# Optimization experiments

Measured on AMD Instinct MI355X. Metric: run time of the kernel, lower is better.

## Reference

```python
import jax, jax.numpy as jnp
import numpy as np

D_MODEL = 1024
HEAD_SIZE = 64

def setup_inputs() -> dict:
    key = jax.random.key(0)
    ks = jax.random.split(key, 7)
    s = 1.0 / np.sqrt(D_MODEL)
    return {
        "x": jax.random.normal(ks[0], (4, 2048, D_MODEL), dtype=jnp.float32),
        "wq": jax.random.uniform(ks[1], (D_MODEL, HEAD_SIZE), jnp.float32, -s, s),
        "bq": jax.random.uniform(ks[2], (HEAD_SIZE,), jnp.float32, -s, s),
        "wk": jax.random.uniform(ks[3], (D_MODEL, HEAD_SIZE), jnp.float32, -s, s),
        "bk": jax.random.uniform(ks[4], (HEAD_SIZE,), jnp.float32, -s, s),
        "wv": jax.random.uniform(ks[5], (D_MODEL, HEAD_SIZE), jnp.float32, -s, s),
        "bv": jax.random.uniform(ks[6], (HEAD_SIZE,), jnp.float32, -s, s),
    }

def reference(x, wq, bq, wk, bk, wv, bv):
    # x: [b, n, d_model]; projections -> [b, n, head_size]
    q = x @ wq + bq
    k = x @ wk + bk
    v = x @ wv + bv
    scores = jnp.einsum("bnd,bmd->bnm", q, k) / jnp.sqrt(jnp.float32(HEAD_SIZE))
    attn = jax.nn.softmax(scores, axis=-1)  # [b, n, n]
    return jnp.einsum("bnm,bmd->bnd", attn, v)
```

## Files before the change

kernel.cpp:

```cpp
#include <hip/hip_runtime.h>
#include <math.h>

#define D_MODEL 1024
#define HEAD 64
#define SEQ 2048
#define BATCH 4

typedef _Float16 f16x4 __attribute__((ext_vector_type(4)));
typedef _Float16 f16x8 __attribute__((ext_vector_type(8)));
typedef float f32x4 __attribute__((ext_vector_type(4)));

__global__ __launch_bounds__(256) void prep_w(
    const float* __restrict__ wq, const float* __restrict__ wk,
    const float* __restrict__ wv, _Float16* __restrict__ wT)
{
    const float* w = (blockIdx.y == 0) ? wq : (blockIdx.y == 1) ? wk : wv;
    const int kbase = blockIdx.x * 64;
    __shared__ float t[64][65];
    const int tid = threadIdx.x;
    #pragma unroll
    for (int i = 0; i < 16; i++) {
        int idx = tid + i * 256;
        int kk = idx >> 6, c = idx & 63;
        t[kk][c] = w[(size_t)(kbase + kk) * 64 + c];
    }
    __syncthreads();
    #pragma unroll
    for (int i = 0; i < 16; i++) {
        int idx = tid + i * 256;
        int c = idx >> 6, kk = idx & 63;
        wT[(size_t)(blockIdx.y * 64 + c) * 1024 + kbase + kk] = (_Float16)t[kk][c];
    }
}

__global__ __launch_bounds__(896, 7) void proj_kernel(
    const float* __restrict__ x, const _Float16* __restrict__ wT,
    const float* __restrict__ bq, const float* __restrict__ bk2,
    const float* __restrict__ bv,
    _Float16* __restrict__ q, _Float16* __restrict__ k, _Float16* __restrict__ vT)
{
    const int tid = threadIdx.x;
    const int wave = tid >> 6;
    const int lane = tid & 63;
    const int l16 = lane & 15;
    const int quad = lane >> 4;
    const int row0 = blockIdx.x * 16;

    __shared__ __align__(16) _Float16 Xs[2][16][136];

    const bool producer = (wave >= 12);

    const int tid2 = tid - 768;
    const int srow = (tid2 >> 3) & 15;
    const int kg = (tid2 & 7) * 16;
    const float* xp = x + (size_t)(row0 + srow) * D_MODEL + kg;

    const _Float16* wp = wT + (size_t)(wave * 16 + l16) * D_MODEL + quad * 8;

    if (producer) {
        float4 f0 = *(const float4*)(xp);
        float4 f1 = *(const float4*)(xp + 4);
        float4 f2 = *(const float4*)(xp + 8);
        float4 f3 = *(const float4*)(xp + 12);
        f16x8 h0, h1;
        h0[0] = (_Float16)f0.x; h0[1] = (_Float16)f0.y;
        h0[2] = (_Float16)f0.z; h0[3] = (_Float16)f0.w;
        h0[4] = (_Float16)f1.x; h0[5] = (_Float16)f1.y;
        h0[6] = (_Float16)f1.z; h0[7] = (_Float16)f1.w;
        h1[0] = (_Float16)f2.x; h1[1] = (_Float16)f2.y;
        h1[2] = (_Float16)f2.z; h1[3] = (_Float16)f2.w;
        h1[4] = (_Float16)f3.x; h1[5] = (_Float16)f3.y;
        h1[6] = (_Float16)f3.z; h1[7] = (_Float16)f3.w;
        *(f16x8*)&Xs[0][srow][kg] = h0;
        *(f16x8*)&Xs[0][srow][kg + 8] = h1;
    }

    f32x4 acc = (f32x4){0.f, 0.f, 0.f, 0.f};

    #pragma unroll 1
    for (int c = 0; c < 8; c++) {
        __syncthreads();
        if (!producer) {
            f16x8 bw0 = *(const f16x8*)(wp + c * 128);
            f16x8 bw1 = *(const f16x8*)(wp + c * 128 + 32);
            f16x8 bw2 = *(const f16x8*)(wp + c * 128 + 64);
            f16x8 bw3 = *(const f16x8*)(wp + c * 128 + 96);
            const int bsel = c & 1;
            f16x8 aX0 = *(const f16x8*)&Xs[bsel][l16][0 * 32 + quad * 8];
            f16x8 aX1 = *(const f16x8*)&Xs[bsel][l16][1 * 32 + quad * 8];
            f16x8 aX2 = *(const f16x8*)&Xs[bsel][l16][2 * 32 + quad * 8];
            f16x8 aX3 = *(const f16x8*)&Xs[bsel][l16][3 * 32 + quad * 8];
            acc = __builtin_amdgcn_mfma_f32_16x16x32_f16(aX0, bw0, acc, 0, 0, 0);
            acc = __builtin_amdgcn_mfma_f32_16x16x32_f16(aX1, bw1, acc, 0, 0, 0);
            acc = __builtin_amdgcn_mfma_f32_16x16x32_f16(aX2, bw2, acc, 0, 0, 0);
            acc = __builtin_amdgcn_mfma_f32_16x16x32_f16(aX3, bw3, acc, 0, 0, 0);
        } else if (c < 7) {
            const float* p = xp + (c + 1) * 128;
            float4 f0 = *(const float4*)(p);
            float4 f1 = *(const float4*)(p + 4);
            float4 f2 = *(const float4*)(p + 8);
            float4 f3 = *(const float4*)(p + 12);
            f16x8 h0, h1;
            h0[0] = (_Float16)f0.x; h0[1] = (_Float16)f0.y;
            h0[2] = (_Float16)f0.z; h0[3] = (_Float16)f0.w;
            h0[4] = (_Float16)f1.x; h0[5] = (_Float16)f1.y;
            h0[6] = (_Float16)f1.z; h0[7] = (_Float16)f1.w;
            h1[0] = (_Float16)f2.x; h1[1] = (_Float16)f2.y;
            h1[2] = (_Float16)f2.z; h1[3] = (_Float16)f2.w;
            h1[4] = (_Float16)f3.x; h1[5] = (_Float16)f3.y;
            h1[6] = (_Float16)f3.z; h1[7] = (_Float16)f3.w;
            const int nb = (c + 1) & 1;
            *(f16x8*)&Xs[nb][srow][kg] = h0;
            *(f16x8*)&Xs[nb][srow][kg + 8] = h1;
        }
    }

    if (!producer) {
        const int g = wave * 16 + l16;
        const int batch = row0 / SEQ;
        const int rbase = row0 + quad * 4;
        if (g < 64) {
            float bias = bq[g];
            #pragma unroll
            for (int r = 0; r < 4; r++)
                q[(size_t)(rbase + r) * HEAD + g] = (_Float16)((acc[r] + bias) * 0.125f);
        } else if (g < 128) {
            float bias = bk2[g - 64];
            #pragma unroll
            for (int r = 0; r < 4; r++)
                k[(size_t)(rbase + r) * HEAD + (g - 64)] = (_Float16)(acc[r] + bias);
        } else {
            float bias = bv[g - 128];
            f16x4 pk;
            #pragma unroll
            for (int r = 0; r < 4; r++) pk[r] = (_Float16)(acc[r] + bias);
            const int seq0 = row0 - batch * SEQ + quad * 4;
            *(f16x4*)(vT + (size_t)(batch * HEAD + (g - 128)) * SEQ + seq0) = pk;
        }
    }
}

__global__ __launch_bounds__(512, 4) void attn_kernel(
    const _Float16* __restrict__ q, const _Float16* __restrict__ k,
    const _Float16* __restrict__ vT, float* __restrict__ out)
{
    const int tid = threadIdx.x;
    const int wave = tid >> 6;
    const int lane = tid & 63;
    const int l16 = lane & 15;
    const int quad = lane >> 4;
    const int b = blockIdx.y;
    const int q0 = blockIdx.x * 16;

    __shared__ __align__(16) char SM[2 * 18432 + 2 * 17408];
    _Float16 (*Ks)[128][72] = (_Float16(*)[128][72])SM;
    _Float16 (*Vs)[64][136] = (_Float16(*)[64][136])(SM + 2 * 18432);
    float (*Oall)[16][68] = (float(*)[16][68])SM;
    __shared__ float Lall[8][16];

    f16x8 bQ[2];
    {
        const _Float16* qp = q + (size_t)(b * SEQ + q0 + l16) * HEAD + quad * 8;
        bQ[0] = *(const f16x8*)qp;
        bQ[1] = *(const f16x8*)(qp + 32);
    }

    f32x4 O[4];
    #pragma unroll
    for (int dt = 0; dt < 4; dt++) O[dt] = (f32x4){0.f, 0.f, 0.f, 0.f};
    float lpart = 0.f;

    const _Float16* kb = k + (size_t)b * SEQ * HEAD;
    const _Float16* vb = vT + (size_t)b * HEAD * SEQ;

    const int krow = tid >> 3, kc8 = (tid & 7) * 8;
    const int vrow = tid >> 4, vc8 = (tid & 15) * 8;
    const _Float16* kg = kb + (size_t)krow * HEAD + kc8;
    const _Float16* vg = vb + (size_t)vrow * SEQ + vc8;

    f16x8 kr0 = *(const f16x8*)kg;
    f16x8 kr1 = *(const f16x8*)(kg + (size_t)64 * HEAD);
    f16x8 vr0 = *(const f16x8*)vg;
    f16x8 vr1 = *(const f16x8*)(vg + (size_t)32 * SEQ);
    *(f16x8*)&Ks[0][krow][kc8] = kr0;
    *(f16x8*)&Ks[0][krow + 64][kc8] = kr1;
    *(f16x8*)&Vs[0][vrow][vc8] = vr0;
    *(f16x8*)&Vs[0][vrow + 32][vc8] = vr1;

    #pragma unroll 1
    for (int c = 0; c < 16; c++) {
        __syncthreads();
        if (c < 15) {
            const int kc2 = (c + 1) * 128;
            kr0 = *(const f16x8*)(kg + (size_t)kc2 * HEAD);
            kr1 = *(const f16x8*)(kg + (size_t)(kc2 + 64) * HEAD);
            vr0 = *(const f16x8*)(vg + kc2);
            vr1 = *(const f16x8*)(vg + (size_t)32 * SEQ + kc2);
        }
        const int bsel = c & 1;
        f16x8 aK0 = *(const f16x8*)&Ks[bsel][wave * 16 + l16][quad * 8];
        f16x8 aK1 = *(const f16x8*)&Ks[bsel][wave * 16 + l16][32 + quad * 8];
        f32x4 st = __builtin_amdgcn_mfma_f32_16x16x32_f16(aK0, bQ[0], (f32x4){0.f, 0.f, 0.f, 0.f}, 0, 0, 0);
        st = __builtin_amdgcn_mfma_f32_16x16x32_f16(aK1, bQ[1], st, 0, 0, 0);

        float p0 = __expf(st[0]);
        float p1 = __expf(st[1]);
        float p2 = __expf(st[2]);
        float p3 = __expf(st[3]);
        lpart += (p0 + p1) + (p2 + p3);
        f16x4 bP;
        bP[0] = (_Float16)p0; bP[1] = (_Float16)p1;
        bP[2] = (_Float16)p2; bP[3] = (_Float16)p3;

        #pragma unroll
        for (int dt = 0; dt < 4; dt++) {
            f16x4 aV = *(const f16x4*)&Vs[bsel][dt * 16 + l16][wave * 16 + quad * 4];
            O[dt] = __builtin_amdgcn_mfma_f32_16x16x16f16(aV, bP, O[dt], 0, 0, 0);
        }
        if (c < 15) {
            *(f16x8*)&Ks[bsel ^ 1][krow][kc8] = kr0;
            *(f16x8*)&Ks[bsel ^ 1][krow + 64][kc8] = kr1;
            *(f16x8*)&Vs[bsel ^ 1][vrow][vc8] = vr0;
            *(f16x8*)&Vs[bsel ^ 1][vrow + 32][vc8] = vr1;
        }
    }
    __syncthreads();

    lpart += __shfl_xor(lpart, 16);
    lpart += __shfl_xor(lpart, 32);
    if (lane < 16) Lall[wave][l16] = lpart;
    #pragma unroll
    for (int dt = 0; dt < 4; dt++)
        #pragma unroll
        for (int r = 0; r < 4; r++)
            Oall[wave][l16][dt * 16 + quad * 4 + r] = O[dt][r];
    __syncthreads();

    {
        int qi = tid >> 5;
        int dd = (tid & 31) * 2;
        float L = 0.f, o0 = 0.f, o1 = 0.f;
        #pragma unroll
        for (int w = 0; w < 8; w++) {
            L += Lall[w][qi];
            o0 += Oall[w][qi][dd];
            o1 += Oall[w][qi][dd + 1];
        }
        float inv = 1.f / L;
        float2 res = make_float2(o0 * inv, o1 * inv);
        *(float2*)(out + (size_t)(b * SEQ + q0 + qi) * HEAD + dd) = res;
    }
}

extern "C" void kernel_launch(void* const* d_in, const int* in_sizes, int n_in,
                              void* d_out, int out_size, void* d_ws, size_t ws_size,
                              hipStream_t stream) {
    const float* x  = (const float*)d_in[0];
    const float* wq = (const float*)d_in[1];
    const float* bq = (const float*)d_in[2];
    const float* wk = (const float*)d_in[3];
    const float* bk = (const float*)d_in[4];
    const float* wv = (const float*)d_in[5];
    const float* bv = (const float*)d_in[6];
    float* out = (float*)d_out;

    const size_t proj_elems = (size_t)BATCH * SEQ * HEAD;
    _Float16* qh = (_Float16*)d_ws;
    _Float16* kh = qh + proj_elems;
    _Float16* vT = kh + proj_elems;
    _Float16* wT = vT + proj_elems;

    prep_w<<<dim3(16, 3), 256, 0, stream>>>(wq, wk, wv, wT);
    proj_kernel<<<dim3(BATCH * SEQ / 16), 896, 0, stream>>>(x, wT, bq, bk, bv, qh, kh, vT);
    attn_kernel<<<dim3(SEQ / 16, BATCH), 512, 0, stream>>>(qh, kh, vT, out);
}
```

Baseline: 127.5 us.

## Stage projection outputs in LDS and store V in blocked tile layout

The projection kernel now writes its Q/K/V results into shared memory first, then issues wide 16-byte coalesced stores instead of scattered 2-byte and 8-byte stores. V is written in a blocked layout of 16-sequence by 64-dim tiles, so the attention kernel loads each V chunk from a contiguous region instead of strided rows of a transposed matrix. This costs two extra barriers and an LDS transpose for V in the projection kernel, and Es reuses the Xs buffer.

```diff
diff --git a/kernel.cpp b/kernel.cpp
--- a/kernel.cpp
+++ b/kernel.cpp
@@ -37,7 +37,7 @@
     const float* __restrict__ x, const _Float16* __restrict__ wT,
     const float* __restrict__ bq, const float* __restrict__ bk2,
     const float* __restrict__ bv,
-    _Float16* __restrict__ q, _Float16* __restrict__ k, _Float16* __restrict__ vT)
+    _Float16* __restrict__ q, _Float16* __restrict__ k, _Float16* __restrict__ vB)
 {
     const int tid = threadIdx.x;
     const int wave = tid >> 6;
@@ -56,6 +56,14 @@
     const float* xp = x + (size_t)(row0 + srow) * D_MODEL + kg;
 
     const _Float16* wp = wT + (size_t)(wave * 16 + l16) * D_MODEL + quad * 8;
+
+    float bias = 0.f, scl = 1.f;
+    const int g = wave * 16 + l16;
+    if (!producer) {
+        if (g < 64)       { bias = bq[g];        scl = 0.125f; }
+        else if (g < 128) { bias = bk2[g - 64]; }
+        else              { bias = bv[g - 128]; }
+    }
 
     if (producer) {
         float4 f0 = *(const float4*)(xp);
@@ -115,34 +123,40 @@
         }
     }
 
+    __syncthreads();
+    _Float16 (*Es)[200] = (_Float16(*)[200])&Xs[0][0][0];
+
     if (!producer) {
-        const int g = wave * 16 + l16;
-        const int batch = row0 / SEQ;
-        const int rbase = row0 + quad * 4;
-        if (g < 64) {
-            float bias = bq[g];
-            #pragma unroll
-            for (int r = 0; r < 4; r++)
-                q[(size_t)(rbase + r) * HEAD + g] = (_Float16)((acc[r] + bias) * 0.125f);
-        } else if (g < 128) {
-            float bias = bk2[g - 64];
-            #pragma unroll
-            for (int r = 0; r < 4; r++)
-                k[(size_t)(rbase + r) * HEAD + (g - 64)] = (_Float16)(acc[r] + bias);
-        } else {
-            float bias = bv[g - 128];
-            f16x4 pk;
-            #pragma unroll
-            for (int r = 0; r < 4; r++) pk[r] = (_Float16)(acc[r] + bias);
-            const int seq0 = row0 - batch * SEQ + quad * 4;
-            *(f16x4*)(vT + (size_t)(batch * HEAD + (g - 128)) * SEQ + seq0) = pk;
-        }
+        #pragma unroll
+        for (int r = 0; r < 4; r++)
+            Es[quad * 4 + r][g] = (_Float16)((acc[r] + bias) * scl);
+    }
+    __syncthreads();
+
+    const int batch = row0 / SEQ;
+    const int sb = (row0 - batch * SEQ) >> 4;
+    if (tid < 128) {
+        int row = tid >> 3, c8 = (tid & 7) * 8;
+        f16x8 v = *(const f16x8*)&Es[row][c8];
+        *(f16x8*)(q + (size_t)(row0 + row) * HEAD + c8) = v;
+    } else if (tid < 256) {
+        int t = tid - 128;
+        int row = t >> 3, c8 = (t & 7) * 8;
+        f16x8 v = *(const f16x8*)&Es[row][64 + c8];
+        *(f16x8*)(k + (size_t)(row0 + row) * HEAD + c8) = v;
+    } else if (tid < 384) {
+        int t = tid - 256;
+        int d = t >> 1, half = (t & 1) * 8;
+        f16x8 v;
+        #pragma unroll
+        for (int j = 0; j < 8; j++) v[j] = Es[half + j][128 + d];
+        *(f16x8*)(vB + ((size_t)(batch * 128 + sb) * 64 + d) * 16 + half) = v;
     }
 }
 
 __global__ __launch_bounds__(512, 4) void attn_kernel(
     const _Float16* __restrict__ q, const _Float16* __restrict__ k,
-    const _Float16* __restrict__ vT, float* __restrict__ out)
+    const _Float16* __restrict__ vB, float* __restrict__ out)
 {
     const int tid = threadIdx.x;
     const int wave = tid >> 6;
@@ -171,21 +185,25 @@
     float lpart = 0.f;
 
     const _Float16* kb = k + (size_t)b * SEQ * HEAD;
-    const _Float16* vb = vT + (size_t)b * HEAD * SEQ;
 
     const int krow = tid >> 3, kc8 = (tid & 7) * 8;
-    const int vrow = tid >> 4, vc8 = (tid & 15) * 8;
     const _Float16* kg = kb + (size_t)krow * HEAD + kc8;
-    const _Float16* vg = vb + (size_t)vrow * SEQ + vc8;
+
+    const int vhalf = (tid & 1) * 8;
+    const int vd = (tid >> 1) & 63;
+    const int vsbl = tid >> 7;
+    const _Float16* vg = vB + (size_t)b * 131072
+                       + (size_t)vsbl * 1024 + (size_t)vd * 16 + vhalf;
+    const int vk0 = vsbl * 16 + vhalf;
 
     f16x8 kr0 = *(const f16x8*)kg;
     f16x8 kr1 = *(const f16x8*)(kg + (size_t)64 * HEAD);
     f16x8 vr0 = *(const f16x8*)vg;
-    f16x8 vr1 = *(const f16x8*)(vg + (size_t)32 * SEQ);
+    f16x8 vr1 = *(const f16x8*)(vg + 4 * 1024);
     *(f16x8*)&Ks[0][krow][kc8] = kr0;
     *(f16x8*)&Ks[0][krow + 64][kc8] = kr1;
-    *(f16x8*)&Vs[0][vrow][vc8] = vr0;
-    *(f16x8*)&Vs[0][vrow + 32][vc8] = vr1;
+    *(f16x8*)&Vs[0][vd][vk0] = vr0;
+    *(f16x8*)&Vs[0][vd][vk0 + 64] = vr1;
 
     #pragma unroll 1
     for (int c = 0; c < 16; c++) {
@@ -194,8 +212,8 @@
             const int kc2 = (c + 1) * 128;
             kr0 = *(const f16x8*)(kg + (size_t)kc2 * HEAD);
             kr1 = *(const f16x8*)(kg + (size_t)(kc2 + 64) * HEAD);
-            vr0 = *(const f16x8*)(vg + kc2);
-            vr1 = *(const f16x8*)(vg + (size_t)32 * SEQ + kc2);
+            vr0 = *(const f16x8*)(vg + (size_t)(c + 1) * 8192);
+            vr1 = *(const f16x8*)(vg + (size_t)(c + 1) * 8192 + 4 * 1024);
         }
         const int bsel = c & 1;
         f16x8 aK0 = *(const f16x8*)&Ks[bsel][wave * 16 + l16][quad * 8];
@@ -220,8 +238,8 @@
         if (c < 15) {
             *(f16x8*)&Ks[bsel ^ 1][krow][kc8] = kr0;
             *(f16x8*)&Ks[bsel ^ 1][krow + 64][kc8] = kr1;
-            *(f16x8*)&Vs[bsel ^ 1][vrow][vc8] = vr0;
-            *(f16x8*)&Vs[bsel ^ 1][vrow + 32][vc8] = vr1;
+            *(f16x8*)&Vs[bsel ^ 1][vd][vk0] = vr0;
+            *(f16x8*)&Vs[bsel ^ 1][vd][vk0 + 64] = vr1;
         }
     }
     __syncthreads();
@@ -267,10 +285,10 @@
     const size_t proj_elems = (size_t)BATCH * SEQ * HEAD;
     _Float16* qh = (_Float16*)d_ws;
     _Float16* kh = qh + proj_elems;
-    _Float16* vT = kh + proj_elems;
-    _Float16* wT = vT + proj_elems;
+    _Float16* vB = kh + proj_elems;
+    _Float16* wT = vB + proj_elems;
 
     prep_w<<<dim3(16, 3), 256, 0, stream>>>(wq, wk, wv, wT);
-    proj_kernel<<<dim3(BATCH * SEQ / 16), 896, 0, stream>>>(x, wT, bq, bk, bv, qh, kh, vT);
-    attn_kernel<<<dim3(SEQ / 16, BATCH), 512, 0, stream>>>(qh, kh, vT, out);
-}
+    proj_kernel<<<dim3(BATCH * SEQ / 16), 896, 0, stream>>>(x, wT, bq, bk, bv, qh, kh, vB);
+    attn_kernel<<<dim3(SEQ / 16, BATCH), 512, 0, stream>>>(qh, kh, vB, out);
+}
```

New measurement: 129.1 us. No clear change (+1.3%).
